# Kernel tuning notes

Measured on AMD Instinct MI355X. Metric: run time of the kernel, lower is better.

Reference implementation:

```python
import jax, jax.numpy as jnp
import numpy as np

B, C, H, W = 8, 32, 120, 160
MAX_ITER = 3
DAMP = 1e-4
OCC_THRES = 0.1

def setup_inputs():
    key = jax.random.key(0)
    ks = jax.random.split(key, 7)
    R = jnp.broadcast_to(jnp.eye(3, dtype=jnp.float32), (B, 3, 3))
    t = 0.01 * jax.random.normal(ks[0], (B, 3), jnp.float32)
    F0 = jax.random.normal(ks[1], (B, C, H, W), jnp.float32)
    F1 = jax.random.normal(ks[2], (B, C, H, W), jnp.float32)
    invD0 = 0.1 + 0.9 * jax.random.uniform(ks[3], (B, 1, H, W), dtype=jnp.float32)
    invD1 = 0.1 + 0.9 * jax.random.uniform(ks[4], (B, 1, H, W), dtype=jnp.float32)
    K = jnp.broadcast_to(jnp.array([150.0, 150.0, (W - 1) / 2.0, (H - 1) / 2.0], jnp.float32), (B, 4))
    sigma0 = jax.random.uniform(ks[5], (B, 1, H, W), dtype=jnp.float32)
    sigma1 = jax.random.uniform(ks[6], (B, 1, H, W), dtype=jnp.float32)
    return {"R": R, "t": t, "F0": F0, "F1": F1, "invD0": invD0, "invD1": invD1,
            "K": K, "sigma0": sigma0, "sigma1": sigma1}

def _sobel_grad(F):
    # Sobel gradient with replicate padding, normalized (feature_gradient)
    b, c, h, w = F.shape
    kx = jnp.array([[-1., 0., 1.], [-2., 0., 2.], [-1., 0., 1.]], F.dtype).reshape(1, 1, 3, 3)
    ky = jnp.array([[-1., -2., -1.], [0., 0., 0.], [1., 2., 1.]], F.dtype).reshape(1, 1, 3, 3)
    Fp = jnp.pad(F.reshape(b * c, 1, h, w), ((0, 0), (0, 0), (1, 1), (1, 1)), mode='edge')
    dn = ('NCHW', 'OIHW', 'NCHW')
    dx = jax.lax.conv_general_dilated(Fp, kx, (1, 1), 'VALID', dimension_numbers=dn)
    dy = jax.lax.conv_general_dilated(Fp, ky, (1, 1), 'VALID', dimension_numbers=dn)
    mag = jnp.sqrt(dx * dx + dy * dy + 1e-8)
    return (dx / mag).reshape(b, c, h, w), (dy / mag).reshape(b, c, h, w)

def _warp_features(F, u, v):
    # bilinear sampling of F [B,C,H,W] at pixel coords u, v [B,1,H,W], border clamp
    b, c, h, w = F.shape
    u = jnp.clip(u.reshape(b, -1), 0.0, w - 1.0)
    v = jnp.clip(v.reshape(b, -1), 0.0, h - 1.0)
    x0 = jnp.floor(u); y0 = jnp.floor(v)
    wx = (u - x0)[:, None, :]; wy = (v - y0)[:, None, :]
    x0i = x0.astype(jnp.int32); y0i = y0.astype(jnp.int32)
    x1i = jnp.minimum(x0i + 1, w - 1); y1i = jnp.minimum(y0i + 1, h - 1)
    Ff = F.reshape(b, c, h * w)
    def g(yi, xi):
        idx = jnp.broadcast_to((yi * w + xi)[:, None, :], (b, c, yi.shape[-1]))
        return jnp.take_along_axis(Ff, idx, axis=2)
    out = (g(y0i, x0i) * (1 - wx) * (1 - wy) + g(y0i, x1i) * wx * (1 - wy)
           + g(y1i, x0i) * (1 - wx) * wy + g(y1i, x1i) * wx * wy)
    return out.reshape(b, c, h, w)

def _xy_grid(K, b, h, w):
    fx, fy, cx, cy = K[:, 0], K[:, 1], K[:, 2], K[:, 3]
    uu, vv = jnp.meshgrid(jnp.arange(w, dtype=K.dtype), jnp.arange(h, dtype=K.dtype))
    px = (uu[None] - cx[:, None, None]) / fx[:, None, None]
    py = (vv[None] - cy[:, None, None]) / fy[:, None, None]
    return px[:, None], py[:, None]  # [B,1,H,W]

def _warp_inverse_depth(px, py, invD, Rm, t, K):
    b, _, h, w = px.shape
    xyz = jnp.concatenate([px, py, jnp.ones_like(px)], axis=1).reshape(b, 3, h * w)
    warped = jnp.matmul(Rm, xyz) + t[:, :, None] * invD.reshape(b, 1, h * w)
    x_, y_, s_ = warped[:, 0], warped[:, 1], warped[:, 2]
    fx, fy, cx, cy = K[:, 0:1], K[:, 1:2], K[:, 2:3], K[:, 3:4]
    u = (x_ / s_) * fx + cx
    v = (y_ / s_) * fy + cy
    inv_z = invD.reshape(b, h * w) / s_
    return u.reshape(b, 1, h, w), v.reshape(b, 1, h, w), inv_z.reshape(b, 1, h, w)

def _jacobian_warping(invD, K, px, py, Rm, t):
    # compute_Jacobian_warping with pose: returns dx_dp, dy_dp each [B,HW,6]
    b, _, h, w = invD.shape
    xyz = jnp.concatenate([px, py, invD], axis=1).reshape(b, 3, h * w)
    warped = jnp.matmul(Rm, xyz) + t[:, :, None]
    x = warped[:, 0][..., None]; y = warped[:, 1][..., None]; iz = warped[:, 2][..., None]
    xy = x * y
    o = jnp.zeros_like(x)
    dx_dp = jnp.concatenate([-xy, 1 + x * x, -y, iz, o, -iz * x], axis=2)
    dy_dp = jnp.concatenate([-1 - y * y, xy, x, o, iz, -iz * y], axis=2)
    fx = K[:, 0].reshape(b, 1, 1); fy = K[:, 1].reshape(b, 1, 1)
    return dx_dp * fx, dy_dp * fy

def _se3_exp(xi):
    # xi [B,6] = [omega(3), v(3)] matching Jacobian column order (rotation first)
    w = xi[:, :3]; v = xi[:, 3:]
    th2 = jnp.sum(w * w, axis=1, keepdims=True)
    th = jnp.sqrt(th2 + 1e-12)
    a = jnp.sin(th) / th
    bb = (1 - jnp.cos(th)) / (th2 + 1e-12)
    cc = (1 - a) / (th2 + 1e-12)
    z = jnp.zeros_like(w[:, 0])
    wx = jnp.stack([z, -w[:, 2], w[:, 1],
                    w[:, 2], z, -w[:, 0],
                    -w[:, 1], w[:, 0], z], axis=1).reshape(-1, 3, 3)
    wx2 = jnp.matmul(wx, wx)
    I = jnp.eye(3, dtype=xi.dtype)[None]
    Rm = I + a[..., None] * wx + bb[..., None] * wx2
    V = I + bb[..., None] * wx + cc[..., None] * wx2
    dt = jnp.matmul(V, v[..., None])[..., 0]
    return Rm, dt

def _forward(R, t, F0, F1, invD0, invD1, K, sigma0, sigma1):
    b, c, h, w = F0.shape
    hw = h * w
    px, py = _xy_grid(K, b, h, w)
    # feature gradient of F1 is pose-independent -> hoisted out of the loop
    JF_x, JF_y = _sobel_grad(F1)
    weights = jnp.ones_like(F0)
    for _ in range(MAX_ITER):
        # --- compute_warped_residual ---
        u, v, inv_z = _warp_inverse_depth(px, py, invD0, R, t, K)
        F1w = _warp_features(F1, u, v)
        invD1w = _warp_features(invD1, u, v)
        inview = (u > 0) & (u < w - 1) & (v > 0) & (v < h - 1)
        occ = ~((inv_z > invD1w - OCC_THRES) & inview)  # [B,1,H,W]
        res = jnp.where(occ, jnp.asarray(0.001, F0.dtype), F1w - F0)  # [B,C,H,W]
        # --- compute_Jacobian (J_p = -dF/dp) ---
        JFxw = _warp_features(JF_x, u, v).reshape(b, c, hw, 1)
        JFyw = _warp_features(JF_y, u, v).reshape(b, c, hw, 1)
        Jx_p, Jy_p = _jacobian_warping(invD0, K, px, py, R, t)  # [B,HW,6]
        J_p = -(JFxw * Jx_p[:, None] + JFyw * Jy_p[:, None]).reshape(b, c * hw, 6)
        # --- robust weights (Cauchy m-estimator stand-in for mEst_func) ---
        weights = 1.0 / (1.0 + res * res)
        # --- damped Gauss-Newton solve (directSolver stand-in) ---
        JtWJ = jnp.einsum('bnk,bnl->bkl', J_p, J_p)
        rhs = jnp.einsum('bnk,bn->bk', J_p, (weights * res).reshape(b, -1))
        A = JtWJ + DAMP * jnp.eye(6, dtype=J_p.dtype)[None]
        dp = jnp.linalg.solve(A, rhs[..., None])[..., 0]
        dR, dt = _se3_exp(dp)
        t = jnp.matmul(dR, t[..., None])[..., 0] + dt
        R = jnp.matmul(dR, R)
    # pack pose + weights into one array: [B, 9 + 3 + C*H*W]
    return jnp.concatenate([R.reshape(b, 9), t, weights.reshape(b, -1)], axis=1)

def reference(R, t, F0, F1, invD0, invD1, K, sigma0, sigma1):
    return _forward(R, t, F0, F1, invD0, invD1, K, sigma0, sigma1)
```

## Files before the change

### kernel.cpp

```cpp
#include <hip/hip_runtime.h>
#include <hip/hip_fp16.h>
#include <math.h>

#define Bn 8
#define Cn 32
#define Hn 120
#define Wn 160
#define HW (Hn*Wn)
#define CHW (Cn*HW)
#define OUTB (12 + CHW)
#define DAMP_C 1e-4
#define OCC_THRES_C 0.1f

#define NCG 2
#define CPG (Cn/NCG)
#define BPB (HW/256)

#define TPX 64
#define NTILE (HW/TPX)

union H8 { ulonglong2 q; __half h[8]; };

__global__ void init_kernel(const float* __restrict__ R_in,
                            const float* __restrict__ t_in,
                            float* __restrict__ pose,
                            float* __restrict__ accum) {
    int b = threadIdx.x;
    if (b < Bn) {
        for (int i = 0; i < 9; ++i) pose[b*12 + i] = R_in[b*9 + i];
        for (int i = 0; i < 3; ++i) pose[b*12 + 9 + i] = t_in[b*3 + i];
        for (int i = 0; i < 32; ++i) accum[b*32 + i] = 0.0f;
    }
}

__global__ __launch_bounds__(256) void prep_kernel(
    const float* __restrict__ F1, const float* __restrict__ F0,
    __half* __restrict__ F1t, __half* __restrict__ F0t,
    __half* __restrict__ Gxt, __half* __restrict__ Gyt)
{
    __shared__ __align__(16) __half sF1[TPX][40];
    __shared__ __align__(16) __half sF0[TPX][40];
    __shared__ __align__(16) __half sGx[TPX][40];
    __shared__ __align__(16) __half sGy[TPX][40];
    int tile = blockIdx.x % NTILE;
    int b    = blockIdx.x / NTILE;
    int p0 = tile * TPX;
    int p_in = threadIdx.x & 63;
    int c0   = threadIdx.x >> 6;
    int p = p0 + p_in;
    int y = p / Wn, x = p % Wn;
    int ym = max(y-1,0)*Wn, yc = y*Wn, yp = min(y+1,Hn-1)*Wn;
    int xm = max(x-1,0), xp = min(x+1,Wn-1);
    H8 rf1, rf0, rgx, rgy;
    #pragma unroll
    for (int k = 0; k < 8; ++k) {
        int c = c0*8 + k;
        const float* Fp = F1 + ((size_t)b*Cn + c)*HW;
        float a00=Fp[ym+xm], a01=Fp[ym+x], a02=Fp[ym+xp];
        float a10=Fp[yc+xm], a11=Fp[yc+x], a12=Fp[yc+xp];
        float a20=Fp[yp+xm], a21=Fp[yp+x], a22=Fp[yp+xp];
        float dx = (a02-a00) + 2.0f*(a12-a10) + (a22-a20);
        float dy = (a20-a00) + 2.0f*(a21-a01) + (a22-a02);
        float mag = sqrtf(dx*dx + dy*dy + 1e-8f);
        rgx.h[k] = __float2half(dx / mag);
        rgy.h[k] = __float2half(dy / mag);
        rf1.h[k] = __float2half(a11);
        rf0.h[k] = __float2half(F0[((size_t)b*Cn + c)*HW + p]);
    }
    *reinterpret_cast<ulonglong2*>(&sF1[p_in][c0*8]) = rf1.q;
    *reinterpret_cast<ulonglong2*>(&sF0[p_in][c0*8]) = rf0.q;
    *reinterpret_cast<ulonglong2*>(&sGx[p_in][c0*8]) = rgx.q;
    *reinterpret_cast<ulonglong2*>(&sGy[p_in][c0*8]) = rgy.q;
    __syncthreads();
    int cq = threadIdx.x >> 7;
    int pi = (threadIdx.x >> 1) & 63;
    int hq = threadIdx.x & 1;
    H8 of1, of0, ogx, ogy;
    int so = cq*16 + hq*8;
    of1.q = *reinterpret_cast<const ulonglong2*>(&sF1[pi][so]);
    of0.q = *reinterpret_cast<const ulonglong2*>(&sF0[pi][so]);
    ogx.q = *reinterpret_cast<const ulonglong2*>(&sGx[pi][so]);
    ogy.q = *reinterpret_cast<const ulonglong2*>(&sGy[pi][so]);
    size_t o = (((size_t)b*NCG + cq)*HW + p0 + pi)*CPG + hq*8;
    *reinterpret_cast<ulonglong2*>(F1t + o) = of1.q;
    *reinterpret_cast<ulonglong2*>(F0t + o) = of0.q;
    *reinterpret_cast<ulonglong2*>(Gxt + o) = ogx.q;
    *reinterpret_cast<ulonglong2*>(Gyt + o) = ogy.q;
}

template<bool LAST>
__global__ __launch_bounds__(256, 2) void accum_kernel(
    const float* __restrict__ invD0, const float* __restrict__ invD1,
    const float* __restrict__ Kin,
    const __half* __restrict__ F1t, const __half* __restrict__ F0t,
    const __half* __restrict__ Gxt, const __half* __restrict__ Gyt,
    const float* __restrict__ pose, float* __restrict__ accum,
    float* __restrict__ out)
{
    __shared__ float sp[16];
    __shared__ float sred[4*27];
    int blk = blockIdx.x;
    int pblk = blk % BPB;
    int cg   = (blk / BPB) % NCG;
    int b    = blk / (BPB * NCG);
    int p = pblk * 256 + threadIdx.x;
    if (threadIdx.x < 12) sp[threadIdx.x] = pose[b*12 + threadIdx.x];
    else if (threadIdx.x < 16) sp[threadIdx.x] = Kin[b*4 + threadIdx.x - 12];
    __syncthreads();
    float R0=sp[0],R1=sp[1],R2=sp[2],R3=sp[3],R4=sp[4],R5=sp[5],R6=sp[6],R7=sp[7],R8=sp[8];
    float t0=sp[9],t1=sp[10],t2=sp[11];
    float fx=sp[12],fy=sp[13],cx=sp[14],cy=sp[15];

    int y = p / Wn, x = p % Wn;
    float px = ((float)x - cx) / fx;
    float py = ((float)y - cy) / fy;
    float d = invD0[(size_t)b*HW + p];

    float X = R0*px + R1*py + R2 + t0*d;
    float Y = R3*px + R4*py + R5 + t1*d;
    float S = R6*px + R7*py + R8 + t2*d;
    float u = X / S * fx + cx;
    float v = Y / S * fy + cy;
    float iz = d / S;
    bool inview = (u > 0.0f) && (u < (float)(Wn-1)) && (v > 0.0f) && (v < (float)(Hn-1));

    float uc = fminf(fmaxf(u, 0.0f), (float)(Wn-1));
    float vc = fminf(fmaxf(v, 0.0f), (float)(Hn-1));
    float x0f = floorf(uc), y0f = floorf(vc);
    float wx = uc - x0f, wy = vc - y0f;
    int x0 = (int)x0f, y0 = (int)y0f;
    int x1 = min(x0+1, Wn-1), y1 = min(y0+1, Hn-1);
    int i00 = y0*Wn + x0, i01 = y0*Wn + x1, i10 = y1*Wn + x0, i11 = y1*Wn + x1;
    float w00 = (1.0f-wx)*(1.0f-wy), w01 = wx*(1.0f-wy);
    float w10 = (1.0f-wx)*wy,        w11 = wx*wy;

    const float* iD1 = invD1 + (size_t)b*HW;
    float invD1w = iD1[i00]*w00 + iD1[i01]*w01 + iD1[i10]*w10 + iD1[i11]*w11;
    bool occ = !((iz > invD1w - OCC_THRES_C) && inview);

    float xj  = R0*px + R1*py + R2*d + t0;
    float yj  = R3*px + R4*py + R5*d + t1;
    float izj = R6*px + R7*py + R8*d + t2;
    float Jx[6], Jy[6];
    Jx[0] = -xj*yj*fx;        Jx[1] = (1.0f + xj*xj)*fx; Jx[2] = -yj*fx;
    Jx[3] = izj*fx;           Jx[4] = 0.0f;              Jx[5] = -izj*xj*fx;
    Jy[0] = -(1.0f + yj*yj)*fy; Jy[1] = xj*yj*fy;        Jy[2] = xj*fy;
    Jy[3] = 0.0f;             Jy[4] = izj*fy;            Jy[5] = -izj*yj*fy;

    size_t gbase = ((size_t)b*NCG + cg)*HW*CPG;
    const __half* F1g = F1t + gbase;
    const __half* F0g = F0t + gbase;
    const __half* Gxg = Gxt + gbase;
    const __half* Gyg = Gyt + gbase;
    size_t t00 = (size_t)i00*CPG, t01 = (size_t)i01*CPG;
    size_t t10 = (size_t)i10*CPG, t11 = (size_t)i11*CPG;
    H8 f00[2], f01[2], f10[2], f11[2], ff0[2];
    H8 gx00[2], gx01[2], gx10[2], gx11[2];
    H8 gy00[2], gy01[2], gy10[2], gy11[2];
    #pragma unroll
    for (int h = 0; h < 2; ++h) {
        f00[h].q  = *reinterpret_cast<const ulonglong2*>(F1g + t00 + h*8);
        f01[h].q  = *reinterpret_cast<const ulonglong2*>(F1g + t01 + h*8);
        f10[h].q  = *reinterpret_cast<const ulonglong2*>(F1g + t10 + h*8);
        f11[h].q  = *reinterpret_cast<const ulonglong2*>(F1g + t11 + h*8);
        gx00[h].q = *reinterpret_cast<const ulonglong2*>(Gxg + t00 + h*8);
        gx01[h].q = *reinterpret_cast<const ulonglong2*>(Gxg + t01 + h*8);
        gx10[h].q = *reinterpret_cast<const ulonglong2*>(Gxg + t10 + h*8);
        gx11[h].q = *reinterpret_cast<const ulonglong2*>(Gxg + t11 + h*8);
        gy00[h].q = *reinterpret_cast<const ulonglong2*>(Gyg + t00 + h*8);
        gy01[h].q = *reinterpret_cast<const ulonglong2*>(Gyg + t01 + h*8);
        gy10[h].q = *reinterpret_cast<const ulonglong2*>(Gyg + t10 + h*8);
        gy11[h].q = *reinterpret_cast<const ulonglong2*>(Gyg + t11 + h*8);
        ff0[h].q  = *reinterpret_cast<const ulonglong2*>(F0g + (size_t)p*CPG + h*8);
    }

    int co = cg * CPG;
    float A2 = 0.0f, B2 = 0.0f, ABc = 0.0f, Sx = 0.0f, Sy = 0.0f;
    #pragma unroll
    for (int cc = 0; cc < CPG; ++cc) {
        int h = cc >> 3, k = cc & 7;
        float f1w = __half2float(f00[h].h[k])*w00 + __half2float(f01[h].h[k])*w01
                  + __half2float(f10[h].h[k])*w10 + __half2float(f11[h].h[k])*w11;
        float gx  = __half2float(gx00[h].h[k])*w00 + __half2float(gx01[h].h[k])*w01
                  + __half2float(gx10[h].h[k])*w10 + __half2float(gx11[h].h[k])*w11;
        float gy  = __half2float(gy00[h].h[k])*w00 + __half2float(gy01[h].h[k])*w01
                  + __half2float(gy10[h].h[k])*w10 + __half2float(gy11[h].h[k])*w11;
        float r = occ ? 0.001f : (f1w - __half2float(ff0[h].h[k]));
        float wt = 1.0f / (1.0f + r*r);
        if (LAST) __builtin_nontemporal_store(wt, &out[(size_t)b*OUTB + 12 + (co+cc)*HW + p]);
        A2 += gx*gx; B2 += gy*gy; ABc += gx*gy;
        float wr = wt * r;
        Sx += wr*gx; Sy += wr*gy;
    }

    float part[27];
    {
        int idx = 0;
        #pragma unroll
        for (int k = 0; k < 6; ++k)
            #pragma unroll
            for (int l = k; l < 6; ++l)
                part[idx++] = A2*Jx[k]*Jx[l] + ABc*(Jx[k]*Jy[l] + Jy[k]*Jx[l]) + B2*Jy[k]*Jy[l];
        #pragma unroll
        for (int k = 0; k < 6; ++k) part[21+k] = -(Sx*Jx[k] + Sy*Jy[k]);
    }

    #pragma unroll
    for (int i = 0; i < 27; ++i) {
        float vsum = part[i];
        for (int off = 32; off > 0; off >>= 1) vsum += __shfl_down(vsum, off, 64);
        part[i] = vsum;
    }
    int lane = threadIdx.x & 63, wave = threadIdx.x >> 6;
    if (lane == 0)
        for (int i = 0; i < 27; ++i) sred[wave*27 + i] = part[i];
    __syncthreads();
    if (threadIdx.x < 27) {
        float s = sred[threadIdx.x] + sred[27+threadIdx.x] + sred[54+threadIdx.x] + sred[81+threadIdx.x];
        atomicAdd(&accum[b*32 + threadIdx.x], s);
    }
}

__global__ void solve_kernel(float* __restrict__ pose, float* __restrict__ accum,
                             float* __restrict__ out, int write_out) {
    int b = threadIdx.x;
    if (b >= Bn) return;
    double A[6][7];
    {
        float acc[27];
        for (int i = 0; i < 27; ++i) acc[i] = accum[b*32 + i];
        int idx = 0;
        for (int k = 0; k < 6; ++k)
            for (int l = k; l < 6; ++l) {
                double vv = (double)acc[idx++];
                A[k][l] = vv; A[l][k] = vv;
            }
        for (int k = 0; k < 6; ++k) { A[k][k] += DAMP_C; A[k][6] = (double)acc[21+k]; }
        for (int i = 0; i < 32; ++i) accum[b*32 + i] = 0.0f;
    }
    for (int col = 0; col < 6; ++col) {
        int piv = col;
        double mx = fabs(A[col][col]);
        for (int r = col+1; r < 6; ++r) { double a = fabs(A[r][col]); if (a > mx) { mx = a; piv = r; } }
        if (piv != col)
            for (int j = col; j < 7; ++j) { double tmp = A[col][j]; A[col][j] = A[piv][j]; A[piv][j] = tmp; }
        double inv = 1.0 / A[col][col];
        for (int r = col+1; r < 6; ++r) {
            double f = A[r][col] * inv;
            for (int j = col; j < 7; ++j) A[r][j] -= f * A[col][j];
        }
    }
    double dp[6];
    for (int col = 5; col >= 0; --col) {
        double s = A[col][6];
        for (int j = col+1; j < 6; ++j) s -= A[col][j] * dp[j];
        dp[col] = s / A[col][col];
    }
    double w0 = dp[0], w1 = dp[1], w2 = dp[2];
    double v0 = dp[3], v1 = dp[4], v2 = dp[5];
    double th2 = w0*w0 + w1*w1 + w2*w2;
    double th = sqrt(th2 + 1e-12);
    float thf = (float)th;
    double sth = (double)sinf(thf);
    double cth = (double)cosf(thf);
    double a = sth / th;
    double bb = (1.0 - cth) / (th2 + 1e-12);
    double cc = (1.0 - a) / (th2 + 1e-12);
    double wxm[3][3] = {{0,-w2,w1},{w2,0,-w0},{-w1,w0,0}};
    double wx2[3][3];
    for (int i = 0; i < 3; ++i)
        for (int j = 0; j < 3; ++j) {
            double s = 0;
            for (int k = 0; k < 3; ++k) s += wxm[i][k]*wxm[k][j];
            wx2[i][j] = s;
        }
    double dR[3][3], V[3][3];
    for (int i = 0; i < 3; ++i)
        for (int j = 0; j < 3; ++j) {
            double I = (i == j) ? 1.0 : 0.0;
            dR[i][j] = I + a*wxm[i][j] + bb*wx2[i][j];
            V[i][j]  = I + bb*wxm[i][j] + cc*wx2[i][j];
        }
    double dt[3];
    for (int i = 0; i < 3; ++i) dt[i] = V[i][0]*v0 + V[i][1]*v1 + V[i][2]*v2;
    double Ro[3][3], to[3];
    for (int i = 0; i < 9; ++i) Ro[i/3][i%3] = (double)pose[b*12 + i];
    for (int i = 0; i < 3; ++i) to[i] = (double)pose[b*12 + 9 + i];
    double tn[3], Rn[3][3];
    for (int i = 0; i < 3; ++i)
        tn[i] = dR[i][0]*to[0] + dR[i][1]*to[1] + dR[i][2]*to[2] + dt[i];
    for (int i = 0; i < 3; ++i)
        for (int j = 0; j < 3; ++j)
            Rn[i][j] = dR[i][0]*Ro[0][j] + dR[i][1]*Ro[1][j] + dR[i][2]*Ro[2][j];
    for (int i = 0; i < 9; ++i) pose[b*12 + i] = (float)Rn[i/3][i%3];
    for (int i = 0; i < 3; ++i) pose[b*12 + 9 + i] = (float)tn[i];
    if (write_out) {
        for (int i = 0; i < 9; ++i) out[(size_t)b*OUTB + i] = (float)Rn[i/3][i%3];
        for (int i = 0; i < 3; ++i) out[(size_t)b*OUTB + 9 + i] = (float)tn[i];
    }
}

extern "C" void kernel_launch(void* const* d_in, const int* in_sizes, int n_in,
                              void* d_out, int out_size, void* d_ws, size_t ws_size,
                              hipStream_t stream) {
    const float* R_in  = (const float*)d_in[0];
    const float* t_in  = (const float*)d_in[1];
    const float* F0    = (const float*)d_in[2];
    const float* F1    = (const float*)d_in[3];
    const float* invD0 = (const float*)d_in[4];
    const float* invD1 = (const float*)d_in[5];
    const float* Kin   = (const float*)d_in[6];
    float* out = (float*)d_out;

    __half* F1t = (__half*)d_ws;
    __half* F0t = F1t + (size_t)Bn*CHW;
    __half* Gxt = F0t + (size_t)Bn*CHW;
    __half* Gyt = Gxt + (size_t)Bn*CHW;
    float* accum = (float*)(Gyt + (size_t)Bn*CHW);
    float* pose  = accum + Bn*32;

    init_kernel<<<1, 64, 0, stream>>>(R_in, t_in, pose, accum);
    prep_kernel<<<Bn*NTILE, 256, 0, stream>>>(F1, F0, F1t, F0t, Gxt, Gyt);

    for (int it = 0; it < 3; ++it) {
        bool last = (it == 2);
        if (last)
            accum_kernel<true><<<Bn*NCG*BPB, 256, 0, stream>>>(
                invD0, invD1, Kin, F1t, F0t, Gxt, Gyt, pose, accum, out);
        else
            accum_kernel<false><<<Bn*NCG*BPB, 256, 0, stream>>>(
                invD0, invD1, Kin, F1t, F0t, Gxt, Gyt, pose, accum, out);
        solve_kernel<<<1, 64, 0, stream>>>(pose, accum, out, last ? 1 : 0);
    }
}
```

Baseline: 212.1 us.

## Fuse init and solve into neighbor kernels; vectorize Sobel loads in prep

The init work moves into block 0 of the prep kernel. The per-iteration 6x6 solve moves into the accumulation kernel: the last block to finish, detected through a global atomic counter, performs it. This cuts the launch count from eight to four. The prep kernel now loads F1 rows as float4 with a 4-pixel-wide stencil per thread instead of nine scalar loads per pixel. The trade-offs are a threadfence and atomic at the tail of every block, a serial solve on a single block, and scattered 2-byte shared-memory stores in prep that may cause bank conflicts.

Measured after the change: 508.8 us. 2.4x slower.

```diff
diff --git a/kernel.cpp b/kernel.cpp
--- a/kernel.cpp
+++ b/kernel.cpp
@@ -21,23 +21,23 @@
 
 union H8 { ulonglong2 q; __half h[8]; };
 
-__global__ void init_kernel(const float* __restrict__ R_in,
-                            const float* __restrict__ t_in,
-                            float* __restrict__ pose,
-                            float* __restrict__ accum) {
-    int b = threadIdx.x;
-    if (b < Bn) {
-        for (int i = 0; i < 9; ++i) pose[b*12 + i] = R_in[b*9 + i];
-        for (int i = 0; i < 3; ++i) pose[b*12 + 9 + i] = t_in[b*3 + i];
-        for (int i = 0; i < 32; ++i) accum[b*32 + i] = 0.0f;
-    }
-}
-
 __global__ __launch_bounds__(256) void prep_kernel(
     const float* __restrict__ F1, const float* __restrict__ F0,
+    const float* __restrict__ R_in, const float* __restrict__ t_in,
     __half* __restrict__ F1t, __half* __restrict__ F0t,
-    __half* __restrict__ Gxt, __half* __restrict__ Gyt)
+    __half* __restrict__ Gxt, __half* __restrict__ Gyt,
+    float* __restrict__ pose, float* __restrict__ accum,
+    unsigned int* __restrict__ counter)
 {
+    if (blockIdx.x == 0) {
+        int b = threadIdx.x;
+        if (b < Bn) {
+            for (int i = 0; i < 9; ++i) pose[b*12 + i] = R_in[b*9 + i];
+            for (int i = 0; i < 3; ++i) pose[b*12 + 9 + i] = t_in[b*3 + i];
+            for (int i = 0; i < 32; ++i) accum[b*32 + i] = 0.0f;
+        }
+        if (threadIdx.x == 0) *counter = 0u;
+    }
     __shared__ __align__(16) __half sF1[TPX][40];
     __shared__ __align__(16) __half sF0[TPX][40];
     __shared__ __align__(16) __half sGx[TPX][40];
@@ -45,38 +45,45 @@
     int tile = blockIdx.x % NTILE;
     int b    = blockIdx.x / NTILE;
     int p0 = tile * TPX;
-    int p_in = threadIdx.x & 63;
-    int c0   = threadIdx.x >> 6;
-    int p = p0 + p_in;
-    int y = p / Wn, x = p % Wn;
+    int xg = threadIdx.x & 15;
+    int cp = threadIdx.x >> 4;
+    int pg = p0 + xg*4;
+    int y = pg / Wn, x = pg % Wn;
     int ym = max(y-1,0)*Wn, yc = y*Wn, yp = min(y+1,Hn-1)*Wn;
-    int xm = max(x-1,0), xp = min(x+1,Wn-1);
-    H8 rf1, rf0, rgx, rgy;
+    int xl = max(x-1,0), xr = min(x+4,Wn-1);
     #pragma unroll
-    for (int k = 0; k < 8; ++k) {
-        int c = c0*8 + k;
+    for (int cc = 0; cc < 2; ++cc) {
+        int c = cp*2 + cc;
         const float* Fp = F1 + ((size_t)b*Cn + c)*HW;
-        float a00=Fp[ym+xm], a01=Fp[ym+x], a02=Fp[ym+xp];
-        float a10=Fp[yc+xm], a11=Fp[yc+x], a12=Fp[yc+xp];
-        float a20=Fp[yp+xm], a21=Fp[yp+x], a22=Fp[yp+xp];
-        float dx = (a02-a00) + 2.0f*(a12-a10) + (a22-a20);
-        float dy = (a20-a00) + 2.0f*(a21-a01) + (a22-a02);
-        float mag = sqrtf(dx*dx + dy*dy + 1e-8f);
-        rgx.h[k] = __float2half(dx / mag);
-        rgy.h[k] = __float2half(dy / mag);
-        rf1.h[k] = __float2half(a11);
-        rf0.h[k] = __float2half(F0[((size_t)b*Cn + c)*HW + p]);
-    }
-    *reinterpret_cast<ulonglong2*>(&sF1[p_in][c0*8]) = rf1.q;
-    *reinterpret_cast<ulonglong2*>(&sF0[p_in][c0*8]) = rf0.q;
-    *reinterpret_cast<ulonglong2*>(&sGx[p_in][c0*8]) = rgx.q;
-    *reinterpret_cast<ulonglong2*>(&sGy[p_in][c0*8]) = rgy.q;
+        float4 r0 = *reinterpret_cast<const float4*>(Fp + ym + x);
+        float4 r1 = *reinterpret_cast<const float4*>(Fp + yc + x);
+        float4 r2 = *reinterpret_cast<const float4*>(Fp + yp + x);
+        float l0 = Fp[ym+xl], q0 = Fp[ym+xr];
+        float l1 = Fp[yc+xl], q1 = Fp[yc+xr];
+        float l2 = Fp[yp+xl], q2 = Fp[yp+xr];
+        float4 f0v = *reinterpret_cast<const float4*>(F0 + ((size_t)b*Cn + c)*HW + pg);
+        float a0[6] = {l0, r0.x, r0.y, r0.z, r0.w, q0};
+        float a1[6] = {l1, r1.x, r1.y, r1.z, r1.w, q1};
+        float a2[6] = {l2, r2.x, r2.y, r2.z, r2.w, q2};
+        float f0a[4] = {f0v.x, f0v.y, f0v.z, f0v.w};
+        #pragma unroll
+        for (int j = 0; j < 4; ++j) {
+            float dx = (a0[j+2]-a0[j]) + 2.0f*(a1[j+2]-a1[j]) + (a2[j+2]-a2[j]);
+            float dy = (a2[j]-a0[j]) + 2.0f*(a2[j+1]-a0[j+1]) + (a2[j+2]-a0[j+2]);
+            float mag = sqrtf(dx*dx + dy*dy + 1e-8f);
+            int px = xg*4 + j;
+            sGx[px][c] = __float2half(dx / mag);
+            sGy[px][c] = __float2half(dy / mag);
+            sF1[px][c] = __float2half(a1[j+1]);
+            sF0[px][c] = __float2half(f0a[j]);
+        }
+    }
     __syncthreads();
     int cq = threadIdx.x >> 7;
     int pi = (threadIdx.x >> 1) & 63;
     int hq = threadIdx.x & 1;
+    int so = cq*16 + hq*8;
     H8 of1, of0, ogx, ogy;
-    int so = cq*16 + hq*8;
     of1.q = *reinterpret_cast<const ulonglong2*>(&sF1[pi][so]);
     of0.q = *reinterpret_cast<const ulonglong2*>(&sF0[pi][so]);
     ogx.q = *reinterpret_cast<const ulonglong2*>(&sGx[pi][so]);
@@ -94,11 +101,13 @@
     const float* __restrict__ Kin,
     const __half* __restrict__ F1t, const __half* __restrict__ F0t,
     const __half* __restrict__ Gxt, const __half* __restrict__ Gyt,
-    const float* __restrict__ pose, float* __restrict__ accum,
+    float* __restrict__ pose, float* __restrict__ accum,
+    unsigned int* __restrict__ counter,
     float* __restrict__ out)
 {
     __shared__ float sp[16];
     __shared__ float sred[4*27];
+    __shared__ unsigned int sdone;
     int blk = blockIdx.x;
     int pblk = blk % BPB;
     int cg   = (blk / BPB) % NCG;
@@ -177,8 +186,8 @@
     int co = cg * CPG;
     float A2 = 0.0f, B2 = 0.0f, ABc = 0.0f, Sx = 0.0f, Sy = 0.0f;
     #pragma unroll
-    for (int cc = 0; cc < CPG; ++cc) {
-        int h = cc >> 3, k = cc & 7;
+    for (int ccv = 0; ccv < CPG; ++ccv) {
+        int h = ccv >> 3, k = ccv & 7;
         float f1w = __half2float(f00[h].h[k])*w00 + __half2float(f01[h].h[k])*w01
                   + __half2float(f10[h].h[k])*w10 + __half2float(f11[h].h[k])*w11;
         float gx  = __half2float(gx00[h].h[k])*w00 + __half2float(gx01[h].h[k])*w01
@@ -187,7 +196,7 @@
                   + __half2float(gy10[h].h[k])*w10 + __half2float(gy11[h].h[k])*w11;
         float r = occ ? 0.001f : (f1w - __half2float(ff0[h].h[k]));
         float wt = 1.0f / (1.0f + r*r);
-        if (LAST) __builtin_nontemporal_store(wt, &out[(size_t)b*OUTB + 12 + (co+cc)*HW + p]);
+        if (LAST) __builtin_nontemporal_store(wt, &out[(size_t)b*OUTB + 12 + (co+ccv)*HW + p]);
         A2 += gx*gx; B2 += gy*gy; ABc += gx*gy;
         float wr = wt * r;
         Sx += wr*gx; Sy += wr*gy;
@@ -219,16 +228,21 @@
         float s = sred[threadIdx.x] + sred[27+threadIdx.x] + sred[54+threadIdx.x] + sred[81+threadIdx.x];
         atomicAdd(&accum[b*32 + threadIdx.x], s);
     }
-}
-
-__global__ void solve_kernel(float* __restrict__ pose, float* __restrict__ accum,
-                             float* __restrict__ out, int write_out) {
-    int b = threadIdx.x;
-    if (b >= Bn) return;
+
+    __threadfence();
+    __syncthreads();
+    if (threadIdx.x == 0) sdone = atomicAdd(counter, 1u);
+    __syncthreads();
+    if (sdone != (unsigned)(gridDim.x - 1)) return;
+    __threadfence();
+    int bb = threadIdx.x;
+    if (bb == 0) atomicExch(counter, 0u);
+    if (bb >= Bn) return;
+    float acc[27];
+    for (int i = 0; i < 27; ++i) acc[i] = atomicAdd(&accum[bb*32 + i], 0.0f);
+    for (int i = 0; i < 27; ++i) atomicExch(&accum[bb*32 + i], 0.0f);
     double A[6][7];
     {
-        float acc[27];
-        for (int i = 0; i < 27; ++i) acc[i] = accum[b*32 + i];
         int idx = 0;
         for (int k = 0; k < 6; ++k)
             for (int l = k; l < 6; ++l) {
@@ -236,7 +250,6 @@
                 A[k][l] = vv; A[l][k] = vv;
             }
         for (int k = 0; k < 6; ++k) { A[k][k] += DAMP_C; A[k][6] = (double)acc[21+k]; }
-        for (int i = 0; i < 32; ++i) accum[b*32 + i] = 0.0f;
     }
     for (int col = 0; col < 6; ++col) {
         int piv = col;
@@ -264,8 +277,8 @@
     double sth = (double)sinf(thf);
     double cth = (double)cosf(thf);
     double a = sth / th;
-    double bb = (1.0 - cth) / (th2 + 1e-12);
-    double cc = (1.0 - a) / (th2 + 1e-12);
+    double bbv = (1.0 - cth) / (th2 + 1e-12);
+    double ccv2 = (1.0 - a) / (th2 + 1e-12);
     double wxm[3][3] = {{0,-w2,w1},{w2,0,-w0},{-w1,w0,0}};
     double wx2[3][3];
     for (int i = 0; i < 3; ++i)
@@ -278,25 +291,25 @@
     for (int i = 0; i < 3; ++i)
         for (int j = 0; j < 3; ++j) {
             double I = (i == j) ? 1.0 : 0.0;
-            dR[i][j] = I + a*wxm[i][j] + bb*wx2[i][j];
-            V[i][j]  = I + bb*wxm[i][j] + cc*wx2[i][j];
+            dR[i][j] = I + a*wxm[i][j] + bbv*wx2[i][j];
+            V[i][j]  = I + bbv*wxm[i][j] + ccv2*wx2[i][j];
         }
     double dt[3];
     for (int i = 0; i < 3; ++i) dt[i] = V[i][0]*v0 + V[i][1]*v1 + V[i][2]*v2;
     double Ro[3][3], to[3];
-    for (int i = 0; i < 9; ++i) Ro[i/3][i%3] = (double)pose[b*12 + i];
-    for (int i = 0; i < 3; ++i) to[i] = (double)pose[b*12 + 9 + i];
+    for (int i = 0; i < 9; ++i) Ro[i/3][i%3] = (double)pose[bb*12 + i];
+    for (int i = 0; i < 3; ++i) to[i] = (double)pose[bb*12 + 9 + i];
     double tn[3], Rn[3][3];
     for (int i = 0; i < 3; ++i)
         tn[i] = dR[i][0]*to[0] + dR[i][1]*to[1] + dR[i][2]*to[2] + dt[i];
     for (int i = 0; i < 3; ++i)
         for (int j = 0; j < 3; ++j)
             Rn[i][j] = dR[i][0]*Ro[0][j] + dR[i][1]*Ro[1][j] + dR[i][2]*Ro[2][j];
-    for (int i = 0; i < 9; ++i) pose[b*12 + i] = (float)Rn[i/3][i%3];
-    for (int i = 0; i < 3; ++i) pose[b*12 + 9 + i] = (float)tn[i];
-    if (write_out) {
-        for (int i = 0; i < 9; ++i) out[(size_t)b*OUTB + i] = (float)Rn[i/3][i%3];
-        for (int i = 0; i < 3; ++i) out[(size_t)b*OUTB + 9 + i] = (float)tn[i];
+    for (int i = 0; i < 9; ++i) pose[bb*12 + i] = (float)Rn[i/3][i%3];
+    for (int i = 0; i < 3; ++i) pose[bb*12 + 9 + i] = (float)tn[i];
+    if (LAST) {
+        for (int i = 0; i < 9; ++i) out[(size_t)bb*OUTB + i] = (float)Rn[i/3][i%3];
+        for (int i = 0; i < 3; ++i) out[(size_t)bb*OUTB + 9 + i] = (float)tn[i];
     }
 }
 
@@ -318,18 +331,15 @@
     __half* Gyt = Gxt + (size_t)Bn*CHW;
     float* accum = (float*)(Gyt + (size_t)Bn*CHW);
     float* pose  = accum + Bn*32;
-
-    init_kernel<<<1, 64, 0, stream>>>(R_in, t_in, pose, accum);
-    prep_kernel<<<Bn*NTILE, 256, 0, stream>>>(F1, F0, F1t, F0t, Gxt, Gyt);
-
-    for (int it = 0; it < 3; ++it) {
-        bool last = (it == 2);
-        if (last)
-            accum_kernel<true><<<Bn*NCG*BPB, 256, 0, stream>>>(
-                invD0, invD1, Kin, F1t, F0t, Gxt, Gyt, pose, accum, out);
-        else
-            accum_kernel<false><<<Bn*NCG*BPB, 256, 0, stream>>>(
-                invD0, invD1, Kin, F1t, F0t, Gxt, Gyt, pose, accum, out);
-        solve_kernel<<<1, 64, 0, stream>>>(pose, accum, out, last ? 1 : 0);
-    }
+    unsigned int* counter = (unsigned int*)(pose + Bn*12);
+
+    prep_kernel<<<Bn*NTILE, 256, 0, stream>>>(F1, F0, R_in, t_in,
+                                              F1t, F0t, Gxt, Gyt,
+                                              pose, accum, counter);
+    accum_kernel<false><<<Bn*NCG*BPB, 256, 0, stream>>>(
+        invD0, invD1, Kin, F1t, F0t, Gxt, Gyt, pose, accum, counter, out);
+    accum_kernel<false><<<Bn*NCG*BPB, 256, 0, stream>>>(
+        invD0, invD1, Kin, F1t, F0t, Gxt, Gyt, pose, accum, counter, out);
+    accum_kernel<true><<<Bn*NCG*BPB, 256, 0, stream>>>(
+        invD0, invD1, Kin, F1t, F0t, Gxt, Gyt, pose, accum, counter, out);
 }
```
